# Performance work log

Hardware: AMD Instinct MI355X
Metric: run time of the kernel (lower is better)

Reference implementation:

```python
import jax, jax.numpy as jnp
import numpy as np

N = 100000
E = 1600000
IN_CH = 128
HEADS = 4
OUT_CH = 32


def setup_inputs() -> dict:
    key = jax.random.key(0)
    k1, k2, k3, k4, k5, k6 = jax.random.split(key, 6)
    x = jax.random.normal(k1, (N, IN_CH), dtype=jnp.float32)
    edge_attr = jax.random.normal(k2, (E,), dtype=jnp.float32)
    edge_index = jax.random.randint(k3, (2, E), 0, N, dtype=jnp.int64)
    # xavier-uniform-ish parameter init
    def xavier(k, shape):
        fan_in, fan_out = shape[-1], shape[-2] if len(shape) > 1 else shape[-1]
        lim = jnp.sqrt(6.0 / (fan_in + fan_out)).astype(jnp.float32)
        return jax.random.uniform(k, shape, jnp.float32, -lim, lim)
    lin_w = xavier(k4, (HEADS * OUT_CH, IN_CH))       # nn.Linear weight [out,in]
    lin_edge_w = xavier(k5, (HEADS * OUT_CH, 1))      # [out,1]
    att = xavier(k6, (1, HEADS, 3 * OUT_CH))
    return {"x": x, "edge_attr": edge_attr, "edge_index": edge_index,
            "lin_w": lin_w, "lin_edge_w": lin_edge_w, "att": att}


def reference(x, edge_attr, edge_index, lin_w, lin_edge_w, att):
    n = x.shape[0]
    # node transform: [N, H, C]
    xh = (x @ lin_w.T).reshape(n, HEADS, OUT_CH)
    # edge transform: [E, H, C]
    eh = (edge_attr[:, None] @ lin_edge_w.T).reshape(-1, HEADS, OUT_CH)
    row, col = edge_index[0], edge_index[1]
    # split att into source/dest/edge parts to avoid materializing cat([x_i,x_j,e])
    att_i, att_j, att_e = jnp.split(att, 3, axis=-1)  # each [1, H, C]
    # per-edge attention logits: [E, H]
    alpha = ((xh[row] * att_i).sum(-1)
             + (xh[col] * att_j).sum(-1)
             + (eh * att_e).sum(-1))
    alpha = jax.nn.leaky_relu(alpha, negative_slope=0.2)
    # segment softmax over destination node (row)
    amax = jax.ops.segment_max(alpha, row, num_segments=n)           # [N, H]
    amax = jnp.where(jnp.isfinite(amax), amax, 0.0)
    ex = jnp.exp(alpha - amax[row])
    den = jax.ops.segment_sum(ex, row, num_segments=n)               # [N, H]
    alpha = ex / (den[row] + 1e-16)
    # weighted message scatter-add: [N, H, C]
    out = jax.ops.segment_sum(alpha[..., None] * xh[col], row, num_segments=n)
    # concat heads
    return out.reshape(n, HEADS * OUT_CH)
```

## Files before the change

kernel.cpp:

```cpp
#include <hip/hip_runtime.h>

#define HEADS 4
#define OUT_CH 32
#define HC 128
#define INC 128
#define CAP 48

typedef __attribute__((ext_vector_type(8))) short bfrag;
typedef __attribute__((ext_vector_type(4))) float ffrag;

union U16 { uint4 u; bfrag f; };

__device__ __forceinline__ unsigned short f2bf(float f) {
  unsigned int u = __float_as_uint(f);
  unsigned int r = (u + 0x7FFFu + ((u >> 16) & 1u)) >> 16;
  return (unsigned short)r;
}

__global__ void prep_kernel(const float* __restrict__ W,
                            const float* __restrict__ lew,
                            const float* __restrict__ att,
                            unsigned short* __restrict__ Wb,
                            float* __restrict__ ce) {
  int tid = threadIdx.x;
#pragma unroll
  for (int t = 0; t < 64; t++) {
    int idx = tid + t * 256;
    Wb[idx] = f2bf(W[idx]);
  }
  if (tid < HEADS) {
    float s = 0.f;
    for (int c = 0; c < OUT_CH; ++c)
      s += lew[tid * OUT_CH + c] * att[tid * 96 + 2 * OUT_CH + c];
    ce[tid] = s;
  }
}

#define APITCH 136
__global__ __launch_bounds__(256) void gemm_build(
    const float* __restrict__ x, const unsigned short* __restrict__ Wb,
    const float* __restrict__ att, const int* __restrict__ ei,
    const float* __restrict__ ea, unsigned short* __restrict__ xhb,
    float* __restrict__ si, float* __restrict__ sj, int* __restrict__ cnt,
    unsigned int* __restrict__ slots, int nrows, int E, int G) {
  __shared__ unsigned short Als[4][16 * APITCH];

  if (blockIdx.x >= G) {
    int e = (blockIdx.x - G) * 256 + threadIdx.x;
    if (e < E) {
      int r = ei[e];
      int c = ei[E + e];
      unsigned int u = __float_as_uint(ea[e]);
      unsigned int word = ((u + 0x10000u) & 0xFFFE0000u) | (unsigned int)c;
      int pos = atomicAdd(&cnt[r], 1);
      if (pos < CAP) slots[(size_t)r * CAP + pos] = word;
    }
    return;
  }

  const int tid = threadIdx.x;
  const int wid = tid >> 6;
  const int lane = tid & 63;
  const int row0 = blockIdx.x * 64 + wid * 16;
  if (row0 >= nrows) return;
  unsigned short* As = &Als[wid][0];

#pragma unroll
  for (int t = 0; t < 8; t++) {
    int idx = t * 64 + lane;
    int r = idx >> 5;
    int q = idx & 31;
    int gr = row0 + r;
    float4 v = make_float4(0.f, 0.f, 0.f, 0.f);
    if (gr < nrows) v = ((const float4*)x)[(size_t)gr * 32 + q];
    unsigned int p0 = ((unsigned int)f2bf(v.y) << 16) | f2bf(v.x);
    unsigned int p1 = ((unsigned int)f2bf(v.w) << 16) | f2bf(v.z);
    *(uint2*)&As[r * APITCH + q * 4] = make_uint2(p0, p1);
  }

  const int m15 = lane & 15;
  const int g = lane >> 4;

  ffrag acc[8];
#pragma unroll
  for (int t = 0; t < 8; t++) acc[t] = (ffrag){0.f, 0.f, 0.f, 0.f};

#pragma unroll
  for (int ks = 0; ks < 4; ks++) {
    U16 a;
    a.u = *(const uint4*)&As[m15 * APITCH + ks * 32 + g * 8];
#pragma unroll
    for (int nt = 0; nt < 8; nt++) {
      U16 b;
      b.u = *(const uint4*)&Wb[(size_t)(nt * 16 + m15) * 128 + ks * 32 + g * 8];
      acc[nt] = __builtin_amdgcn_mfma_f32_16x16x32_bf16(a.f, b.f, acc[nt],
                                                        0, 0, 0);
    }
  }

  float ai[8], aj[8];
#pragma unroll
  for (int t = 0; t < 8; t++) {
    int h = t >> 1, c = (t & 1) * 16 + m15;
    ai[t] = att[h * 96 + c];
    aj[t] = att[h * 96 + 32 + c];
  }
#pragma unroll
  for (int reg = 0; reg < 4; reg++) {
    float ph_i[4], ph_j[4];
#pragma unroll
    for (int h = 0; h < 4; h++) {
      ph_i[h] = acc[2 * h][reg] * ai[2 * h] + acc[2 * h + 1][reg] * ai[2 * h + 1];
      ph_j[h] = acc[2 * h][reg] * aj[2 * h] + acc[2 * h + 1][reg] * aj[2 * h + 1];
    }
#pragma unroll
    for (int off = 8; off >= 1; off >>= 1) {
#pragma unroll
      for (int h = 0; h < 4; h++) {
        ph_i[h] += __shfl_down(ph_i[h], off, 16);
        ph_j[h] += __shfl_down(ph_j[h], off, 16);
      }
    }
    int gr = row0 + g * 4 + reg;
    if (m15 == 0 && gr < nrows) {
#pragma unroll
      for (int h = 0; h < 4; h++) {
        si[(size_t)gr * 4 + h] = ph_i[h];
        sj[(size_t)gr * 4 + h] = ph_j[h];
      }
    }
  }

#pragma unroll
  for (int t = 0; t < 8; t++) {
#pragma unroll
    for (int reg = 0; reg < 4; reg++) {
      int r = g * 4 + reg;
      int n = t * 16 + m15;
      As[r * 128 + n] = f2bf(acc[t][reg]);
    }
  }
  const uint4* src = (const uint4*)As;
#pragma unroll
  for (int t = 0; t < 4; t++) {
    int idx = t * 64 + lane;
    int r = idx >> 4, q = idx & 15;
    int gr = row0 + r;
    if (gr < nrows) ((uint4*)(xhb + (size_t)gr * 128))[q] = src[idx];
  }
}

__global__ __launch_bounds__(256) void gather_kernel(
    const int* __restrict__ cnt, const unsigned int* __restrict__ slots,
    const float* __restrict__ si, const float* __restrict__ sj,
    const float* __restrict__ ce, const unsigned short* __restrict__ xhb,
    float* __restrict__ out, int n) {
  int node = blockIdx.x * 4 + (threadIdx.x >> 6);
  if (node >= n) return;
  int lane = threadIdx.x & 63;
  int h = lane >> 4;
  float4 si4 = *(const float4*)(si + (size_t)node * 4);
  float4 ce4 = *(const float4*)ce;
  int m = cnt[node];
  if (m > CAP) m = CAP;
  const unsigned int* sl = slots + (size_t)node * CAP;

  int q = lane & 15;
  int kq = q >> 2;
  int hq = q & 3;
  float si_q = hq == 0 ? si4.x : (hq == 1 ? si4.y : (hq == 2 ? si4.z : si4.w));
  float ce_q = hq == 0 ? ce4.x : (hq == 1 ? ce4.y : (hq == 2 ? ce4.z : ce4.w));

  float acc0 = 0.f, acc1 = 0.f, wsum = 0.f;
  int i = 0;
  for (; i + 4 <= m; i += 4) {
    uint4 ww = *(const uint4*)(sl + i);
    unsigned int wsel =
        kq == 0 ? ww.x : (kq == 1 ? ww.y : (kq == 2 ? ww.z : ww.w));
    int cq = wsel & 0x1FFFF;
    float t = si_q + sj[(size_t)cq * 4 + hq] +
              __uint_as_float(wsel & 0xFFFE0000u) * ce_q;
    t = t > 0.f ? t : 0.2f * t;
    float wq = __expf(t);
    float w0 = __shfl(wq, h);
    float w1 = __shfl(wq, 4 + h);
    float w2 = __shfl(wq, 8 + h);
    float w3 = __shfl(wq, 12 + h);
    int c0 = ww.x & 0x1FFFF, c1 = ww.y & 0x1FFFF;
    int c2 = ww.z & 0x1FFFF, c3 = ww.w & 0x1FFFF;
    unsigned int x0 = *(const unsigned int*)(xhb + (size_t)c0 * 128 + lane * 2);
    unsigned int x1 = *(const unsigned int*)(xhb + (size_t)c1 * 128 + lane * 2);
    unsigned int x2 = *(const unsigned int*)(xhb + (size_t)c2 * 128 + lane * 2);
    unsigned int x3 = *(const unsigned int*)(xhb + (size_t)c3 * 128 + lane * 2);
    acc0 += w0 * __uint_as_float(x0 << 16) + w1 * __uint_as_float(x1 << 16) +
            w2 * __uint_as_float(x2 << 16) + w3 * __uint_as_float(x3 << 16);
    acc1 += w0 * __uint_as_float(x0 & 0xFFFF0000u) +
            w1 * __uint_as_float(x1 & 0xFFFF0000u) +
            w2 * __uint_as_float(x2 & 0xFFFF0000u) +
            w3 * __uint_as_float(x3 & 0xFFFF0000u);
    wsum += w0 + w1 + w2 + w3;
  }
  float si_h = h == 0 ? si4.x : (h == 1 ? si4.y : (h == 2 ? si4.z : si4.w));
  float ce_h = h == 0 ? ce4.x : (h == 1 ? ce4.y : (h == 2 ? ce4.z : ce4.w));
  for (; i < m; ++i) {
    unsigned int w = sl[i];
    int c0 = w & 0x1FFFF;
    float t0 = si_h + sj[(size_t)c0 * 4 + h] +
               __uint_as_float(w & 0xFFFE0000u) * ce_h;
    t0 = t0 > 0.f ? t0 : 0.2f * t0;
    float w0 = __expf(t0);
    unsigned int x0 = *(const unsigned int*)(xhb + (size_t)c0 * 128 + lane * 2);
    acc0 += w0 * __uint_as_float(x0 << 16);
    acc1 += w0 * __uint_as_float(x0 & 0xFFFF0000u);
    wsum += w0;
  }
  float inv = 1.0f / (wsum + 1e-16f);
  float2 o;
  o.x = acc0 * inv;
  o.y = acc1 * inv;
  *(float2*)(out + (size_t)node * HC + lane * 2) = o;
}

extern "C" void kernel_launch(void* const* d_in, const int* in_sizes, int n_in,
                              void* d_out, int out_size, void* d_ws,
                              size_t ws_size, hipStream_t stream) {
  const float* x = (const float*)d_in[0];
  const float* edge_attr = (const float*)d_in[1];
  const int* ei = (const int*)d_in[2];
  const float* lin_w = (const float*)d_in[3];
  const float* lew = (const float*)d_in[4];
  const float* att = (const float*)d_in[5];
  float* out = (float*)d_out;

  const int N = in_sizes[0] / INC;
  const int E = in_sizes[1];

  unsigned int* slots = (unsigned int*)d_ws;
  unsigned short* xhb = (unsigned short*)(slots + (size_t)N * CAP);
  float* si = (float*)(xhb + (size_t)N * 128);
  float* sj = si + (size_t)N * 4;
  float* ce = sj + (size_t)N * 4;
  unsigned short* Wb = (unsigned short*)(ce + 16);
  int* cnt = (int*)(Wb + 16384);

  hipMemsetAsync(cnt, 0, (size_t)N * sizeof(int), stream);
  prep_kernel<<<1, 256, 0, stream>>>(lin_w, lew, att, Wb, ce);

  const int G = (N + 63) / 64;
  const int B = (E + 255) / 256;
  gemm_build<<<G + B, 256, 0, stream>>>(x, Wb, att, ei, edge_attr, xhb, si,
                                        sj, cnt, slots, N, E, G);
  gather_kernel<<<(N + 3) / 4, 256, 0, stream>>>(cnt, slots, si, sj, ce, xhb,
                                                 out, N);
}
```

Baseline: 296.2 us.

## Batch edge binning atomics, pad counters, compute per-head logits without shuffles

Result: slower. 308.2 us (+4.1%).

```diff
diff --git a/kernel.cpp b/kernel.cpp
--- a/kernel.cpp
+++ b/kernel.cpp
@@ -5,6 +5,7 @@
 #define HC 128
 #define INC 128
 #define CAP 48
+#define CSTRIDE 16
 
 typedef __attribute__((ext_vector_type(8))) short bfrag;
 typedef __attribute__((ext_vector_type(4))) float ffrag;
@@ -46,15 +47,27 @@
   __shared__ unsigned short Als[4][16 * APITCH];
 
   if (blockIdx.x >= G) {
-    int e = (blockIdx.x - G) * 256 + threadIdx.x;
-    if (e < E) {
-      int r = ei[e];
-      int c = ei[E + e];
-      unsigned int u = __float_as_uint(ea[e]);
-      unsigned int word = ((u + 0x10000u) & 0xFFFE0000u) | (unsigned int)c;
-      int pos = atomicAdd(&cnt[r], 1);
-      if (pos < CAP) slots[(size_t)r * CAP + pos] = word;
-    }
+    int base = (blockIdx.x - G) * 1024 + threadIdx.x;
+    int r[4];
+    unsigned int wd[4];
+    bool act[4];
+#pragma unroll
+    for (int t = 0; t < 4; t++) {
+      int e = base + t * 256;
+      act[t] = e < E;
+      int ee = act[t] ? e : 0;
+      r[t] = ei[ee];
+      unsigned int c = (unsigned int)ei[E + ee];
+      unsigned int u = __float_as_uint(ea[ee]);
+      wd[t] = ((u + 0x10000u) & 0xFFFE0000u) | c;
+    }
+    int pos[4];
+#pragma unroll
+    for (int t = 0; t < 4; t++)
+      if (act[t]) pos[t] = atomicAdd(&cnt[r[t] * CSTRIDE], 1);
+#pragma unroll
+    for (int t = 0; t < 4; t++)
+      if (act[t] && pos[t] < CAP) slots[(size_t)r[t] * CAP + pos[t]] = wd[t];
     return;
   }
 
@@ -159,35 +172,31 @@
   if (node >= n) return;
   int lane = threadIdx.x & 63;
   int h = lane >> 4;
-  float4 si4 = *(const float4*)(si + (size_t)node * 4);
-  float4 ce4 = *(const float4*)ce;
-  int m = cnt[node];
+  float si_h = si[(size_t)node * 4 + h];
+  float ce_h = ce[h];
+  int m = cnt[(size_t)node * CSTRIDE];
   if (m > CAP) m = CAP;
   const unsigned int* sl = slots + (size_t)node * CAP;
-
-  int q = lane & 15;
-  int kq = q >> 2;
-  int hq = q & 3;
-  float si_q = hq == 0 ? si4.x : (hq == 1 ? si4.y : (hq == 2 ? si4.z : si4.w));
-  float ce_q = hq == 0 ? ce4.x : (hq == 1 ? ce4.y : (hq == 2 ? ce4.z : ce4.w));
 
   float acc0 = 0.f, acc1 = 0.f, wsum = 0.f;
   int i = 0;
   for (; i + 4 <= m; i += 4) {
     uint4 ww = *(const uint4*)(sl + i);
-    unsigned int wsel =
-        kq == 0 ? ww.x : (kq == 1 ? ww.y : (kq == 2 ? ww.z : ww.w));
-    int cq = wsel & 0x1FFFF;
-    float t = si_q + sj[(size_t)cq * 4 + hq] +
-              __uint_as_float(wsel & 0xFFFE0000u) * ce_q;
-    t = t > 0.f ? t : 0.2f * t;
-    float wq = __expf(t);
-    float w0 = __shfl(wq, h);
-    float w1 = __shfl(wq, 4 + h);
-    float w2 = __shfl(wq, 8 + h);
-    float w3 = __shfl(wq, 12 + h);
     int c0 = ww.x & 0x1FFFF, c1 = ww.y & 0x1FFFF;
     int c2 = ww.z & 0x1FFFF, c3 = ww.w & 0x1FFFF;
+    float t0 = si_h + sj[(size_t)c0 * 4 + h] +
+               __uint_as_float(ww.x & 0xFFFE0000u) * ce_h;
+    float t1 = si_h + sj[(size_t)c1 * 4 + h] +
+               __uint_as_float(ww.y & 0xFFFE0000u) * ce_h;
+    float t2 = si_h + sj[(size_t)c2 * 4 + h] +
+               __uint_as_float(ww.z & 0xFFFE0000u) * ce_h;
+    float t3 = si_h + sj[(size_t)c3 * 4 + h] +
+               __uint_as_float(ww.w & 0xFFFE0000u) * ce_h;
+    t0 = t0 > 0.f ? t0 : 0.2f * t0;
+    t1 = t1 > 0.f ? t1 : 0.2f * t1;
+    t2 = t2 > 0.f ? t2 : 0.2f * t2;
+    t3 = t3 > 0.f ? t3 : 0.2f * t3;
+    float w0 = __expf(t0), w1 = __expf(t1), w2 = __expf(t2), w3 = __expf(t3);
     unsigned int x0 = *(const unsigned int*)(xhb + (size_t)c0 * 128 + lane * 2);
     unsigned int x1 = *(const unsigned int*)(xhb + (size_t)c1 * 128 + lane * 2);
     unsigned int x2 = *(const unsigned int*)(xhb + (size_t)c2 * 128 + lane * 2);
@@ -200,8 +209,6 @@
             w3 * __uint_as_float(x3 & 0xFFFF0000u);
     wsum += w0 + w1 + w2 + w3;
   }
-  float si_h = h == 0 ? si4.x : (h == 1 ? si4.y : (h == 2 ? si4.z : si4.w));
-  float ce_h = h == 0 ? ce4.x : (h == 1 ? ce4.y : (h == 2 ? ce4.z : ce4.w));
   for (; i < m; ++i) {
     unsigned int w = sl[i];
     int c0 = w & 0x1FFFF;
@@ -243,11 +250,11 @@
   unsigned short* Wb = (unsigned short*)(ce + 16);
   int* cnt = (int*)(Wb + 16384);
 
-  hipMemsetAsync(cnt, 0, (size_t)N * sizeof(int), stream);
+  hipMemsetAsync(cnt, 0, (size_t)N * CSTRIDE * sizeof(int), stream);
   prep_kernel<<<1, 256, 0, stream>>>(lin_w, lew, att, Wb, ce);
 
   const int G = (N + 63) / 64;
-  const int B = (E + 255) / 256;
+  const int B = (E + 1023) / 1024;
   gemm_build<<<G + B, 256, 0, stream>>>(x, Wb, att, ei, edge_attr, xhb, si,
                                         sj, cnt, slots, N, E, G);
   gather_kernel<<<(N + 3) / 4, 256, 0, stream>>>(cnt, slots, si, sj, ce, xhb,
```
